# Kernel optimization log

Measured on AMD Instinct MI355X. Metric: run time of the kernel, lower is better.

Reference implementation:

```python
import jax, jax.numpy as jnp
import numpy as np

B, T, D, H = 4, 2048, 512, 8
K = D // H  # head dim = 64

def setup_inputs() -> dict:
    key = jax.random.key(0)
    k1, k2, k3, k4 = jax.random.split(key, 4)
    x = jax.random.normal(k1, (B, T, D), dtype=jnp.float32)
    # torch nn.Linear stores weight as [out_features, in_features]
    w_qkv = jax.random.normal(k2, (3 * D, D), dtype=jnp.float32) * (D ** -0.5)
    w_proj = jax.random.normal(k3, (D, D), dtype=jnp.float32) * (D ** -0.5)
    b_proj = jax.random.normal(k4, (D,), dtype=jnp.float32) * 0.01
    return {"x": x, "w_qkv": w_qkv, "w_proj": w_proj, "b_proj": b_proj}

def reference(x, w_qkv, w_proj, b_proj):
    Bx, Tx, Dx = x.shape
    # qkv projection (no bias): [B,T,3D]
    qkv = jnp.einsum('btd,ed->bte', x, w_qkv)
    q, k, v = jnp.split(qkv, 3, axis=-1)
    # [B,H,T,K]
    def heads(t):
        return t.reshape(Bx, Tx, H, K).transpose(0, 2, 1, 3)
    q, k, v = heads(q), heads(k), heads(v)
    # scaled scores with causal mask
    scores = jnp.einsum('bhqk,bhsk->bhqs', q, k) * (K ** -0.5)  # [B,H,T,T]
    causal = jnp.tril(jnp.ones((Tx, Tx), dtype=bool))
    scores = jnp.where(causal, scores, -jnp.inf)
    attn = jax.nn.softmax(scores, axis=-1)  # dropout p=0.0 -> identity
    out = jnp.einsum('bhqs,bhsk->bhqk', attn, v)  # [B,H,T,K]
    out = out.transpose(0, 2, 1, 3).reshape(Bx, Tx, Dx)
    out = jnp.einsum('btd,ed->bte', out, w_proj) + b_proj
    return out
```

## Files before the change

### kernel.cpp

```cpp
#include <hip/hip_runtime.h>
#include <hip/hip_bf16.h>


typedef unsigned short u16;
typedef __attribute__((ext_vector_type(8))) __bf16 bf16x8;
typedef __attribute__((ext_vector_type(8))) unsigned short u16x8;
typedef __attribute__((ext_vector_type(4))) unsigned short u16x4;
typedef __attribute__((ext_vector_type(4))) float f32x4;
typedef __attribute__((ext_vector_type(4))) unsigned u32x4;
typedef __attribute__((ext_vector_type(2))) unsigned u32x2;

#define DEV static __device__ __forceinline__

DEV void async16(const u16* g, u16* l) {
  __builtin_amdgcn_global_load_lds(
      (const __attribute__((address_space(1))) unsigned int*)g,
      (__attribute__((address_space(3))) unsigned int*)l, 16, 0, 0);
}
DEV u16x8 gld8(const u16* p) { return *(const u16x8*)p; }
DEV void lst8(u16* p, u16x8 v) { *(u16x8*)p = v; }
DEV bf16x8 ldsld8(const u16* p) {
  return __builtin_bit_cast(bf16x8, *(const u16x8*)p);
}
DEV f32x4 mfma16(bf16x8 a, bf16x8 b, f32x4 c) {
  return __builtin_amdgcn_mfma_f32_16x16x32_bf16(a, b, c, 0, 0, 0);
}
DEV u16 f2b(float f) {
  unsigned u = __builtin_bit_cast(unsigned, f);
  u += 0x7FFFu + ((u >> 16) & 1u);
  return (u16)(u >> 16);
}
DEV unsigned pk2(float x, float y) {
  __hip_bfloat162 t = __float22bfloat162_rn(float2{x, y});
  unsigned r;
  __builtin_memcpy(&r, &t, 4);
  return r;
}
DEV u16x8 pack8(f32x4 a, f32x4 b) {
  u32x4 t;
  t[0] = pk2(a[0], a[1]);
  t[1] = pk2(a[2], a[3]);
  t[2] = pk2(b[0], b[1]);
  t[3] = pk2(b[2], b[3]);
  return __builtin_bit_cast(u16x8, t);
}

__global__ void cvt_all(const float* __restrict__ x, const float* __restrict__ wq,
                        u16* __restrict__ xb, u16* __restrict__ wqb) {
  constexpr long NX = 8192L * 512 / 8;
  constexpr long NQ = 1536L * 512 / 8;
  const long i = (long)blockIdx.x * 256 + threadIdx.x;
  if (i < NX) {
    const float* p = x + i * 8;
    *(u16x8*)(xb + i * 8) = pack8(*(const f32x4*)p, *(const f32x4*)(p + 4));
  } else if (i < NX + NQ) {
    const long j = i - NX;
    const float* p = wq + j * 8;
    *(u16x8*)(wqb + j * 8) = pack8(*(const f32x4*)p, *(const f32x4*)(p + 4));
  }
}

__global__ void gemm_bb(const u16* __restrict__ A, const u16* __restrict__ Bt,
                        u16* __restrict__ qk, u16* __restrict__ vT, int K) {
  __shared__ __align__(16) u16 As[2][128 * 32];
  __shared__ __align__(16) u16 Bs[2][128 * 32];

  const int t = threadIdx.x, lane = t & 63, w = t >> 6;
  const int lane15 = lane & 15, quad = lane >> 4;
  const int wr = w >> 1, wc = w & 1;

  const int i = blockIdx.x;
  const int rt = (i & 7) | (((i >> 3) & 7) << 3);
  const int ct = i >> 6;
  const long row0 = (long)rt * 128;
  const int col0 = ct * 128;

  const int srow = w * 16 + (lane >> 2);
  const int scol = (lane & 3) * 8;
  const u16* Ag = A + (row0 + srow) * (long)K + scol;
  const u16* Bg = Bt + ((long)col0 + srow) * (long)K + scol;

  f32x4 acc[4][4];
#pragma unroll
  for (int ii = 0; ii < 4; ii++)
#pragma unroll
    for (int j = 0; j < 4; j++) acc[ii][j] = (f32x4)(0.0f);

  for (int k0 = 0; k0 < K; k0 += 64) {
    __syncthreads();
#pragma unroll
    for (int r = 0; r < 2; r++)
#pragma unroll
      for (int hf = 0; hf < 2; hf++) {
        async16(Ag + (long)r * 64 * K + k0 + hf * 32,
                &As[hf][(r * 64 + w * 16) * 32]);
        async16(Bg + (long)r * 64 * K + k0 + hf * 32,
                &Bs[hf][(r * 64 + w * 16) * 32]);
      }
    __syncthreads();

#pragma unroll
    for (int hf = 0; hf < 2; hf++) {
      bf16x8 a[4], b[4];
#pragma unroll
      for (int ii = 0; ii < 4; ii++)
        a[ii] = ldsld8(&As[hf][(wr * 64 + ii * 16 + lane15) * 32 + quad * 8]);
#pragma unroll
      for (int j = 0; j < 4; j++)
        b[j] = ldsld8(&Bs[hf][(wc * 64 + j * 16 + lane15) * 32 + quad * 8]);
#pragma unroll
      for (int ii = 0; ii < 4; ii++)
#pragma unroll
        for (int j = 0; j < 4; j++) acc[ii][j] = mfma16(a[ii], b[j], acc[ii][j]);
    }
  }

  if (col0 >= 1024) {
#pragma unroll
    for (int ii = 0; ii < 4; ii++)
#pragma unroll
      for (int j = 0; j < 4; j++) {
        const int hd = col0 - 1024 + wc * 64 + j * 16 + lane15;
        const long row = row0 + wr * 64 + ii * 16 + quad * 4;
        const long bb = row >> 11;
        const int s = (int)(row & 2047);
        const int ps = (s & ~31) | (((s >> 2) & 3) << 3) | (((s >> 4) & 1) << 2);
        u32x2 pr;
        pr[0] = pk2(acc[ii][j][0], acc[ii][j][1]);
        pr[1] = pk2(acc[ii][j][2], acc[ii][j][3]);
        *(u16x4*)(vT + (bb * 512 + hd) * 2048 + ps) =
            __builtin_bit_cast(u16x4, pr);
      }
  } else {
#pragma unroll
    for (int ii = 0; ii < 4; ii++)
#pragma unroll
      for (int j = 0; j < 4; j++) {
        const int col = col0 + wc * 64 + j * 16 + lane15;
        const float sc = (col < 512) ? 0.18033688f : 1.0f;
#pragma unroll
        for (int r = 0; r < 4; r++) {
          const long row = row0 + wr * 64 + ii * 16 + quad * 4 + r;
          qk[row * 1024 + col] = f2b(acc[ii][j][r] * sc);
        }
      }
  }
}

__global__ void gemm_b64(const u16* __restrict__ A, const float* __restrict__ Bt,
                         const float* __restrict__ bias, float* __restrict__ C,
                         int N, int K) {
  __shared__ __align__(16) u16 As[2][128 * 32];
  __shared__ __align__(16) u16 Bs[2][64 * 32];

  const int t = threadIdx.x, lane = t & 63, w = t >> 6;
  const int lane15 = lane & 15, quad = lane >> 4;
  const int wr = w >> 1, wc = w & 1;

  const int i = blockIdx.x;
  const int rt = (i & 7) | (((i >> 3) & 7) << 3);
  const int ct = i >> 6;
  const long row0 = (long)rt * 128;
  const int col0 = ct * 64;

  const int srow = w * 16 + (lane >> 2);
  const int scol = (lane & 3) * 8;
  const u16* Ag = A + (row0 + srow) * (long)K + scol;

  const int brow = t >> 2, bc = (t & 3) * 16;
  const float* Bg = Bt + (long)(col0 + brow) * K + bc;
  u16* BsD = &Bs[bc >> 5][brow * 32 + (bc & 31)];

  f32x4 acc[4][2];
#pragma unroll
  for (int ii = 0; ii < 4; ii++)
#pragma unroll
    for (int j = 0; j < 2; j++) acc[ii][j] = (f32x4)(0.0f);

  f32x4 q0 = *(const f32x4*)Bg, q1 = *(const f32x4*)(Bg + 4);
  f32x4 q2 = *(const f32x4*)(Bg + 8), q3 = *(const f32x4*)(Bg + 12);

  for (int k0 = 0; k0 < K; k0 += 64) {
    __syncthreads();
#pragma unroll
    for (int r = 0; r < 2; r++)
#pragma unroll
      for (int hf = 0; hf < 2; hf++)
        async16(Ag + (long)r * 64 * K + k0 + hf * 32,
                &As[hf][(r * 64 + w * 16) * 32]);
    lst8(BsD, pack8(q0, q1));
    lst8(BsD + 8, pack8(q2, q3));
    __syncthreads();

    {
      const int kp = (k0 + 64 < K) ? k0 + 64 : k0;
      q0 = *(const f32x4*)(Bg + kp);     q1 = *(const f32x4*)(Bg + kp + 4);
      q2 = *(const f32x4*)(Bg + kp + 8); q3 = *(const f32x4*)(Bg + kp + 12);
    }

#pragma unroll
    for (int hf = 0; hf < 2; hf++) {
      bf16x8 a[4], b[2];
#pragma unroll
      for (int ii = 0; ii < 4; ii++)
        a[ii] = ldsld8(&As[hf][(wr * 64 + ii * 16 + lane15) * 32 + quad * 8]);
#pragma unroll
      for (int j = 0; j < 2; j++)
        b[j] = ldsld8(&Bs[hf][(wc * 32 + j * 16 + lane15) * 32 + quad * 8]);
#pragma unroll
      for (int ii = 0; ii < 4; ii++)
#pragma unroll
        for (int j = 0; j < 2; j++) acc[ii][j] = mfma16(a[ii], b[j], acc[ii][j]);
    }
  }

#pragma unroll
  for (int ii = 0; ii < 4; ii++)
#pragma unroll
    for (int j = 0; j < 2; j++) {
      const int col = col0 + wc * 32 + j * 16 + lane15;
      const float bv = bias[col];
#pragma unroll
      for (int r = 0; r < 4; r++) {
        const long row = row0 + wr * 64 + ii * 16 + quad * 4 + r;
        C[row * (long)N + col] = acc[ii][j][r] + bv;
      }
    }
}

__global__ void attn_v7(const u16* __restrict__ qk, const u16* __restrict__ vT,
                        u16* __restrict__ out) {
  constexpr int T = 2048, LDQ = 1024;
  __shared__ __align__(16) u16 Ks[2][64 * 72];
  __shared__ __align__(16) u16 Vs[2][64 * 72];

  const int t = threadIdx.x, lane = t & 63, w = t >> 6;
  const int lane15 = lane & 15, quad = lane >> 4;

  const int i = blockIdx.x;
  int qb = i & 31;
  if (i >= 512) qb = 31 - qb;
  const int h = (i >> 5) & 7;
  const int b = (i >> 8) & 3;
  const long baseq = (long)b * T * LDQ;
  const u16* vTb = vT + ((long)b * 512 + h * 64) * 2048;

  const u16* gq =
      qk + baseq + (long)(qb * 64 + w * 16 + lane15) * LDQ + h * 64 + quad * 8;
  const bf16x8 qa0 = __builtin_bit_cast(bf16x8, *(const u16x8*)gq);
  const bf16x8 qa1 = __builtin_bit_cast(bf16x8, *(const u16x8*)(gq + 32));

  const int srow = t >> 3, sc8 = (t & 7) * 8;
  const int nsb = qb + 1;

  u16x8 kr0, kr1, vr0, vr1;
  {
    const u16* gk = qk + baseq + (long)srow * LDQ + 512 + h * 64 + sc8;
    kr0 = gld8(gk); kr1 = gld8(gk + (long)32 * LDQ);
    const u16* gv = vTb + (long)srow * 2048 + sc8;
    vr0 = gld8(gv); vr1 = gld8(gv + (long)32 * 2048);
  }
  lst8(&Ks[0][srow * 72 + sc8], kr0);
  lst8(&Ks[0][(srow + 32) * 72 + sc8], kr1);
  lst8(&Vs[0][srow * 72 + sc8], vr0);
  lst8(&Vs[0][(srow + 32) * 72 + sc8], vr1);
  {
    const int sp = (nsb > 1) ? 1 : 0;
    const u16* gk =
        qk + baseq + (long)(sp * 64 + srow) * LDQ + 512 + h * 64 + sc8;
    kr0 = gld8(gk); kr1 = gld8(gk + (long)32 * LDQ);
    const u16* gv = vTb + (long)srow * 2048 + sp * 64 + sc8;
    vr0 = gld8(gv); vr1 = gld8(gv + (long)32 * 2048);
  }

  float lpl = 0.0f;
  f32x4 o[4];
#pragma unroll
  for (int j = 0; j < 4; j++) o[j] = (f32x4)(0.0f);

  const int qin = w * 16 + lane15;

  for (int sb = 0; sb < nsb; ++sb) {
    const u16* Kc = Ks[sb & 1];
    const u16* Vc = Vs[sb & 1];
    u16* Kn = Ks[(sb + 1) & 1];
    u16* Vn = Vs[(sb + 1) & 1];

    __syncthreads();

    lst8(&Kn[srow * 72 + sc8], kr0);
    lst8(&Kn[(srow + 32) * 72 + sc8], kr1);
    lst8(&Vn[srow * 72 + sc8], vr0);
    lst8(&Vn[(srow + 32) * 72 + sc8], vr1);

    {
      const int sp = (sb + 2 < nsb) ? sb + 2 : nsb - 1;
      const u16* gk =
          qk + baseq + (long)(sp * 64 + srow) * LDQ + 512 + h * 64 + sc8;
      kr0 = gld8(gk); kr1 = gld8(gk + (long)32 * LDQ);
      const u16* gv = vTb + (long)srow * 2048 + sp * 64 + sc8;
      vr0 = gld8(gv); vr1 = gld8(gv + (long)32 * 2048);
    }

    f32x4 sf[4];
#pragma unroll
    for (int j = 0; j < 4; j++) {
      f32x4 z = (f32x4)(0.0f);
      z = mfma16(ldsld8(&Kc[(j * 16 + lane15) * 72 + quad * 8]), qa0, z);
      sf[j] = mfma16(ldsld8(&Kc[(j * 16 + lane15) * 72 + quad * 8 + 32]), qa1, z);
    }

    if (sb == qb) {
#pragma unroll
      for (int j = 0; j < 4; j++)
#pragma unroll
        for (int r = 0; r < 4; r++) {
          float p = exp2f(sf[j][r]);
          if (j * 16 + quad * 4 + r > qin) p = 0.0f;
          sf[j][r] = p;
          lpl += p;
        }
    } else {
#pragma unroll
      for (int j = 0; j < 4; j++)
#pragma unroll
        for (int r = 0; r < 4; r++) {
          const float p = exp2f(sf[j][r]);
          sf[j][r] = p;
          lpl += p;
        }
    }

    u32x4 pw0, pw1;
    pw0[0] = pk2(sf[0][0], sf[0][1]); pw0[1] = pk2(sf[0][2], sf[0][3]);
    pw0[2] = pk2(sf[1][0], sf[1][1]); pw0[3] = pk2(sf[1][2], sf[1][3]);
    pw1[0] = pk2(sf[2][0], sf[2][1]); pw1[1] = pk2(sf[2][2], sf[2][3]);
    pw1[2] = pk2(sf[3][0], sf[3][1]); pw1[3] = pk2(sf[3][2], sf[3][3]);
    const bf16x8 pa0 = __builtin_bit_cast(bf16x8, pw0);
    const bf16x8 pa1 = __builtin_bit_cast(bf16x8, pw1);

#pragma unroll
    for (int j = 0; j < 4; j++) {
      const int d0 = (j * 16 + lane15) * 72;
      o[j] = mfma16(pa0, ldsld8(&Vc[d0 + quad * 8]), o[j]);
      o[j] = mfma16(pa1, ldsld8(&Vc[d0 + quad * 8 + 32]), o[j]);
    }
  }

  lpl += __shfl_xor(lpl, 16);
  lpl += __shfl_xor(lpl, 32);

  const long orow0 = (long)b * T + qb * 64 + w * 16;
  float inv[4];
#pragma unroll
  for (int r = 0; r < 4; r++) inv[r] = 1.0f / __shfl(lpl, quad * 4 + r);
#pragma unroll
  for (int j = 0; j < 4; j++)
#pragma unroll
    for (int r = 0; r < 4; r++)
      out[(orow0 + quad * 4 + r) * 512 + h * 64 + j * 16 + lane15] =
          f2b(o[j][r] * inv[r]);
}

extern "C" void kernel_launch(void* const* d_in, const int* in_sizes, int n_in,
                              void* d_out, int out_size, void* d_ws, size_t ws_size,
                              hipStream_t stream) {
  const float* x      = (const float*)d_in[0];
  const float* w_qkv  = (const float*)d_in[1];
  const float* w_proj = (const float*)d_in[2];
  const float* b_proj = (const float*)d_in[3];
  float* out = (float*)d_out;

  u16* qk = (u16*)d_ws;
  u16* vT = qk + (size_t)8192 * 1024;
  u16* xb = vT + (size_t)4 * 512 * 2048;
  u16* wqb = (u16*)d_out;

  cvt_all<<<2432, 256, 0, stream>>>(x, w_qkv, xb, wqb);
  gemm_bb<<<768, 256, 0, stream>>>(xb, wqb, qk, vT, 512);
  attn_v7<<<1024, 256, 0, stream>>>(qk, vT, xb);
  gemm_b64<<<512, 256, 0, stream>>>(xb, w_proj, b_proj, out, 512, 512);
}
```

Measured before the change: 150.1 us.

## Enlarge attention query tile to 128 rows with 32 rows per wave

The attention kernel now processes 128 query rows per block instead of 64, with each wave handling two 16-row query sub-tiles. Each K/V tile staged in shared memory is reused across twice as many queries, halving K/V global traffic and block count. Waves skip key tiles beyond their causal diagonal, the row sums are computed with an MFMA against a ones vector instead of shuffles, and s_setprio raises priority around the compute section. In exchange there are fewer blocks (512) and more registers per thread, which can lower occupancy, and waves in a block do uneven work near the diagonal.

Result: slower. 153.7 us (+2.4%).

```diff
diff --git a/kernel.cpp b/kernel.cpp
--- a/kernel.cpp
+++ b/kernel.cpp
@@ -228,7 +228,7 @@
     }
 }
 
-__global__ void attn_v7(const u16* __restrict__ qk, const u16* __restrict__ vT,
+__global__ void attn_v8(const u16* __restrict__ qk, const u16* __restrict__ vT,
                         u16* __restrict__ out) {
   constexpr int T = 2048, LDQ = 1024;
   __shared__ __align__(16) u16 Ks[2][64 * 72];
@@ -238,47 +238,46 @@
   const int lane15 = lane & 15, quad = lane >> 4;
 
   const int i = blockIdx.x;
-  int qb = i & 31;
-  if (i >= 512) qb = 31 - qb;
-  const int h = (i >> 5) & 7;
-  const int b = (i >> 8) & 3;
+  int qb = i & 15;
+  if (i >= 256) qb = 15 - qb;
+  const int h = (i >> 4) & 7;
+  const int b = (i >> 7) & 3;
   const long baseq = (long)b * T * LDQ;
   const u16* vTb = vT + ((long)b * 512 + h * 64) * 2048;
 
   const u16* gq =
-      qk + baseq + (long)(qb * 64 + w * 16 + lane15) * LDQ + h * 64 + quad * 8;
+      qk + baseq + (long)(qb * 128 + w * 32 + lane15) * LDQ + h * 64 + quad * 8;
   const bf16x8 qa0 = __builtin_bit_cast(bf16x8, *(const u16x8*)gq);
   const bf16x8 qa1 = __builtin_bit_cast(bf16x8, *(const u16x8*)(gq + 32));
+  const bf16x8 qc0 = __builtin_bit_cast(bf16x8, *(const u16x8*)(gq + 16 * LDQ));
+  const bf16x8 qc1 =
+      __builtin_bit_cast(bf16x8, *(const u16x8*)(gq + 16 * LDQ + 32));
 
   const int srow = t >> 3, sc8 = (t & 7) * 8;
-  const int nsb = qb + 1;
+  const int nsb = 2 * qb + 2;
+  const int sbd = 2 * qb + (w >> 1);
+
+  const u16* gk = qk + baseq + (long)srow * LDQ + 512 + h * 64 + sc8;
+  const u16* gv = vTb + (long)srow * 2048 + sc8;
 
   u16x8 kr0, kr1, vr0, vr1;
-  {
-    const u16* gk = qk + baseq + (long)srow * LDQ + 512 + h * 64 + sc8;
-    kr0 = gld8(gk); kr1 = gld8(gk + (long)32 * LDQ);
-    const u16* gv = vTb + (long)srow * 2048 + sc8;
-    vr0 = gld8(gv); vr1 = gld8(gv + (long)32 * 2048);
-  }
+  kr0 = gld8(gk); kr1 = gld8(gk + (long)32 * LDQ);
+  vr0 = gld8(gv); vr1 = gld8(gv + (long)32 * 2048);
   lst8(&Ks[0][srow * 72 + sc8], kr0);
   lst8(&Ks[0][(srow + 32) * 72 + sc8], kr1);
   lst8(&Vs[0][srow * 72 + sc8], vr0);
   lst8(&Vs[0][(srow + 32) * 72 + sc8], vr1);
-  {
-    const int sp = (nsb > 1) ? 1 : 0;
-    const u16* gk =
-        qk + baseq + (long)(sp * 64 + srow) * LDQ + 512 + h * 64 + sc8;
-    kr0 = gld8(gk); kr1 = gld8(gk + (long)32 * LDQ);
-    const u16* gv = vTb + (long)srow * 2048 + sp * 64 + sc8;
-    vr0 = gld8(gv); vr1 = gld8(gv + (long)32 * 2048);
-  }
-
-  float lpl = 0.0f;
-  f32x4 o[4];
-#pragma unroll
-  for (int j = 0; j < 4; j++) o[j] = (f32x4)(0.0f);
-
-  const int qin = w * 16 + lane15;
+  gk += (long)64 * LDQ;
+  gv += 64;
+  kr0 = gld8(gk); kr1 = gld8(gk + (long)32 * LDQ);
+  vr0 = gld8(gv); vr1 = gld8(gv + (long)32 * 2048);
+
+  f32x4 o0[4], o1[4], lsum0 = (f32x4)(0.0f), lsum1 = (f32x4)(0.0f);
+#pragma unroll
+  for (int j = 0; j < 4; j++) { o0[j] = (f32x4)(0.0f); o1[j] = (f32x4)(0.0f); }
+
+  const bf16x8 ones = __builtin_bit_cast(bf16x8, (u16x8)((u16)0x3F80));
+  const int ql0 = ((w & 1) << 5) + lane15;
 
   for (int sb = 0; sb < nsb; ++sb) {
     const u16* Kc = Ks[sb & 1];
@@ -293,73 +292,82 @@
     lst8(&Vn[srow * 72 + sc8], vr0);
     lst8(&Vn[(srow + 32) * 72 + sc8], vr1);
 
-    {
-      const int sp = (sb + 2 < nsb) ? sb + 2 : nsb - 1;
-      const u16* gk =
-          qk + baseq + (long)(sp * 64 + srow) * LDQ + 512 + h * 64 + sc8;
-      kr0 = gld8(gk); kr1 = gld8(gk + (long)32 * LDQ);
-      const u16* gv = vTb + (long)srow * 2048 + sp * 64 + sc8;
-      vr0 = gld8(gv); vr1 = gld8(gv + (long)32 * 2048);
-    }
-
-    f32x4 sf[4];
-#pragma unroll
-    for (int j = 0; j < 4; j++) {
-      f32x4 z = (f32x4)(0.0f);
-      z = mfma16(ldsld8(&Kc[(j * 16 + lane15) * 72 + quad * 8]), qa0, z);
-      sf[j] = mfma16(ldsld8(&Kc[(j * 16 + lane15) * 72 + quad * 8 + 32]), qa1, z);
-    }
-
-    if (sb == qb) {
+    if (sb + 2 < nsb) { gk += (long)64 * LDQ; gv += 64; }
+    kr0 = gld8(gk); kr1 = gld8(gk + (long)32 * LDQ);
+    vr0 = gld8(gv); vr1 = gld8(gv + (long)32 * 2048);
+
+    if (sb <= sbd) {
+      __builtin_amdgcn_s_setprio(1);
+      f32x4 s0[4], s1[4];
+#pragma unroll
+      for (int j = 0; j < 4; j++) {
+        const bf16x8 k0 = ldsld8(&Kc[(j * 16 + lane15) * 72 + quad * 8]);
+        const bf16x8 k1 = ldsld8(&Kc[(j * 16 + lane15) * 72 + quad * 8 + 32]);
+        s0[j] = mfma16(k1, qa1, mfma16(k0, qa0, (f32x4)(0.0f)));
+        s1[j] = mfma16(k1, qc1, mfma16(k0, qc0, (f32x4)(0.0f)));
+      }
+
 #pragma unroll
       for (int j = 0; j < 4; j++)
 #pragma unroll
         for (int r = 0; r < 4; r++) {
-          float p = exp2f(sf[j][r]);
-          if (j * 16 + quad * 4 + r > qin) p = 0.0f;
-          sf[j][r] = p;
-          lpl += p;
+          s0[j][r] = exp2f(s0[j][r]);
+          s1[j][r] = exp2f(s1[j][r]);
         }
-    } else {
-#pragma unroll
-      for (int j = 0; j < 4; j++)
-#pragma unroll
-        for (int r = 0; r < 4; r++) {
-          const float p = exp2f(sf[j][r]);
-          sf[j][r] = p;
-          lpl += p;
-        }
-    }
-
-    u32x4 pw0, pw1;
-    pw0[0] = pk2(sf[0][0], sf[0][1]); pw0[1] = pk2(sf[0][2], sf[0][3]);
-    pw0[2] = pk2(sf[1][0], sf[1][1]); pw0[3] = pk2(sf[1][2], sf[1][3]);
-    pw1[0] = pk2(sf[2][0], sf[2][1]); pw1[1] = pk2(sf[2][2], sf[2][3]);
-    pw1[2] = pk2(sf[3][0], sf[3][1]); pw1[3] = pk2(sf[3][2], sf[3][3]);
-    const bf16x8 pa0 = __builtin_bit_cast(bf16x8, pw0);
-    const bf16x8 pa1 = __builtin_bit_cast(bf16x8, pw1);
-
-#pragma unroll
-    for (int j = 0; j < 4; j++) {
-      const int d0 = (j * 16 + lane15) * 72;
-      o[j] = mfma16(pa0, ldsld8(&Vc[d0 + quad * 8]), o[j]);
-      o[j] = mfma16(pa1, ldsld8(&Vc[d0 + quad * 8 + 32]), o[j]);
-    }
-  }
-
-  lpl += __shfl_xor(lpl, 16);
-  lpl += __shfl_xor(lpl, 32);
-
-  const long orow0 = (long)b * T + qb * 64 + w * 16;
-  float inv[4];
-#pragma unroll
-  for (int r = 0; r < 4; r++) inv[r] = 1.0f / __shfl(lpl, quad * 4 + r);
+      if (sb == sbd) {
+#pragma unroll
+        for (int j = 0; j < 4; j++)
+#pragma unroll
+          for (int r = 0; r < 4; r++) {
+            const int sl = j * 16 + quad * 4 + r;
+            if (sl > ql0) s0[j][r] = 0.0f;
+            if (sl > ql0 + 16) s1[j][r] = 0.0f;
+          }
+      }
+
+      u32x4 w0, w1, w2, w3;
+      w0[0] = pk2(s0[0][0], s0[0][1]); w0[1] = pk2(s0[0][2], s0[0][3]);
+      w0[2] = pk2(s0[1][0], s0[1][1]); w0[3] = pk2(s0[1][2], s0[1][3]);
+      w1[0] = pk2(s0[2][0], s0[2][1]); w1[1] = pk2(s0[2][2], s0[2][3]);
+      w1[2] = pk2(s0[3][0], s0[3][1]); w1[3] = pk2(s0[3][2], s0[3][3]);
+      w2[0] = pk2(s1[0][0], s1[0][1]); w2[1] = pk2(s1[0][2], s1[0][3]);
+      w2[2] = pk2(s1[1][0], s1[1][1]); w2[3] = pk2(s1[1][2], s1[1][3]);
+      w3[0] = pk2(s1[2][0], s1[2][1]); w3[1] = pk2(s1[2][2], s1[2][3]);
+      w3[2] = pk2(s1[3][0], s1[3][1]); w3[3] = pk2(s1[3][2], s1[3][3]);
+      const bf16x8 pa0 = __builtin_bit_cast(bf16x8, w0);
+      const bf16x8 pa1 = __builtin_bit_cast(bf16x8, w1);
+      const bf16x8 pc0 = __builtin_bit_cast(bf16x8, w2);
+      const bf16x8 pc1 = __builtin_bit_cast(bf16x8, w3);
+
+#pragma unroll
+      for (int j = 0; j < 4; j++) {
+        const int d0 = (j * 16 + lane15) * 72;
+        const bf16x8 v0 = ldsld8(&Vc[d0 + quad * 8]);
+        const bf16x8 v1 = ldsld8(&Vc[d0 + quad * 8 + 32]);
+        o0[j] = mfma16(pa1, v1, mfma16(pa0, v0, o0[j]));
+        o1[j] = mfma16(pc1, v1, mfma16(pc0, v0, o1[j]));
+      }
+      lsum0 = mfma16(pa1, ones, mfma16(pa0, ones, lsum0));
+      lsum1 = mfma16(pc1, ones, mfma16(pc0, ones, lsum1));
+      __builtin_amdgcn_s_setprio(0);
+    }
+  }
+
+  const long orow0 = (long)b * T + qb * 128 + w * 32;
+  f32x4 inv0, inv1;
+#pragma unroll
+  for (int r = 0; r < 4; r++) {
+    inv0[r] = 1.0f / lsum0[r];
+    inv1[r] = 1.0f / lsum1[r];
+  }
 #pragma unroll
   for (int j = 0; j < 4; j++)
 #pragma unroll
-    for (int r = 0; r < 4; r++)
-      out[(orow0 + quad * 4 + r) * 512 + h * 64 + j * 16 + lane15] =
-          f2b(o[j][r] * inv[r]);
+    for (int r = 0; r < 4; r++) {
+      const long rr = orow0 + quad * 4 + r;
+      out[rr * 512 + h * 64 + j * 16 + lane15] = f2b(o0[j][r] * inv0[r]);
+      out[(rr + 16) * 512 + h * 64 + j * 16 + lane15] = f2b(o1[j][r] * inv1[r]);
+    }
 }
 
 extern "C" void kernel_launch(void* const* d_in, const int* in_sizes, int n_in,
@@ -378,6 +386,6 @@
 
   cvt_all<<<2432, 256, 0, stream>>>(x, w_qkv, xb, wqb);
   gemm_bb<<<768, 256, 0, stream>>>(xb, wqb, qk, vT, 512);
-  attn_v7<<<1024, 256, 0, stream>>>(qk, vT, xb);
+  attn_v8<<<512, 256, 0, stream>>>(qk, vT, xb);
   gemm_b64<<<512, 256, 0, stream>>>(xb, w_proj, b_proj, out, 512, 512);
 }
```
